# Performance work log

Hardware: AMD Instinct MI355X
Metric: run time of the kernel (lower is better)

## Reference

```python
import jax, jax.numpy as jnp
import numpy as np

N, E, NFEAT, NHID, NCLASS = 50000, 800000, 8, 128, 112
SMOOTH = 0.5          # smoo init arg
NEG_SLOPE_ATT = 0.2   # LeakyReLU slope inside sparse attention (SpGAT convention)
NEG_SLOPE_OUT = 0.01  # F.leaky_relu default in the outer loop
EPS = 1e-16


def setup_inputs() -> dict:
    key = jax.random.key(0)
    ks = jax.random.split(key, 12)
    g = lambda k, shape, s=0.1: jax.random.normal(k, shape, dtype=jnp.float32) * s
    return {
        "x": jax.random.normal(ks[0], (N, NFEAT), dtype=jnp.float32),
        "edge_index": jax.random.randint(ks[1], (2, E), 0, N, dtype=jnp.int64) if jax.config.jax_enable_x64 else jax.random.randint(ks[1], (2, E), 0, N, dtype=jnp.int32),
        "edge_weight": jax.random.uniform(ks[2], (E,), dtype=jnp.float32),
        # ScattterAttentionLayer 1: nfeat -> nhid (weight W, attention vector a split into src/dst halves)
        "W1": g(ks[3], (NFEAT, NHID)),
        "a1_src": g(ks[4], (NHID,)),
        "a1_dst": g(ks[5], (NHID,)),
        # ScattterAttentionLayer 2: nhid -> nhid
        "W2": g(ks[6], (NHID, NHID)),
        "a2_src": g(ks[7], (NHID,)),
        "a2_dst": g(ks[8], (NHID,)),
        # shared BatchNorm1d(nhid)
        "gamma": jnp.ones((NHID,), jnp.float32),
        "beta": jnp.zeros((NHID,), jnp.float32),
        # GC_withres: nhid -> nclass
        "Wg": g(ks[9], (NHID, NCLASS)),
        "bg": jnp.zeros((NCLASS,), jnp.float32),
    }


def scatter_attention(h_in, W, a_src, a_dst, src, dst):
    """Sparse GAT-style scatter attention (SpGraphAttentionLayer math).
    score_ij = exp(-leakyrelu(a_src.h_i + a_dst.h_j)); softmax-normalized per dst node."""
    h = h_in @ W                                   # [N, F]
    f_src = h @ a_src                              # [N]
    f_dst = h @ a_dst                              # [N]
    e = jnp.exp(-jax.nn.leaky_relu(f_src[src] + f_dst[dst], NEG_SLOPE_ATT))  # [E]
    denom = jax.ops.segment_sum(e, dst, num_segments=N) + EPS                # [N]
    num = jax.ops.segment_sum(e[:, None] * h[src], dst, num_segments=N)      # [N, F]
    return num / denom[:, None]


def batchnorm(x, gamma, beta):
    mu = x.mean(axis=0)
    var = x.var(axis=0)
    return (x - mu) * jax.lax.rsqrt(var + 1e-5) * gamma + beta


def reference(x, edge_index, edge_weight, W1, a1_src, a1_dst, W2, a2_src, a2_dst, gamma, beta, Wg, bg):
    src, dst = edge_index[0], edge_index[1]
    # conv loop (nlayers=3 -> two ScattterAttentionLayer convs), shared bn1, leaky_relu; dropout=identity (eval)
    h = scatter_attention(x, W1, a1_src, a1_dst, src, dst)
    h = jax.nn.leaky_relu(batchnorm(h, gamma, beta), NEG_SLOPE_OUT)
    h = scatter_attention(h, W2, a2_src, a2_dst, src, dst)
    h = jax.nn.leaky_relu(batchnorm(h, gamma, beta), NEG_SLOPE_OUT)
    # GC_withres: spmm((smooth*A + I)/(1+smooth), h @ Wg) + bias
    support = h @ Wg                               # [N, nclass]
    w = (SMOOTH / (1.0 + SMOOTH)) * edge_weight    # [E]
    agg = jax.ops.segment_sum(w[:, None] * support[src], dst, num_segments=N)
    return agg + support / (1.0 + SMOOTH) + bg
```

## Files before the change

### kernel.cpp

```cpp
#include <hip/hip_runtime.h>
#include <hip/hip_bf16.h>

#define N_NODES 50000
#define N_EDGES 800000
#define NFEAT   8
#define NHID    128
#define NCLASS  112
#define SEG_EPS 1e-16f
#define BN_EPS  1e-5f
#define CAP     64
#define MACRO_TILES 782
#define NODE_RANGE 6250
#define FILL_CHUNK 2048
#define FILL_CHUNKS 391
#define ATTN_BLOCKS 3125
#define ATTN_ITERS 4
#define Y1_BLOCKS 256

typedef __hip_bfloat16 bf16;
typedef __attribute__((ext_vector_type(8))) short short8;
typedef __attribute__((ext_vector_type(4))) float f32x4;

__device__ __forceinline__ float bfbits2f(unsigned int lo16) {
    union { unsigned int u; float f; } c; c.u = lo16 << 16; return c.f;
}

__device__ __forceinline__ unsigned int pack_bf2(float a, float b) {
    union { unsigned int u; bf16 h[2]; } t;
    t.h[0] = __float2bfloat16(a);
    t.h[1] = __float2bfloat16(b);
    return t.u;
}

__global__ __launch_bounds__(256)
void k_fill_bucket(const int* __restrict__ src, const int* __restrict__ dst,
                   const float* __restrict__ ewt,
                   int* __restrict__ cnt, unsigned int* __restrict__ bucket) {
    const int range = blockIdx.x & 7;
    const int chunk = blockIdx.x >> 3;
    const int lo = range * NODE_RANGE, hi = lo + NODE_RANGE;
    const int e0 = chunk * FILL_CHUNK + threadIdx.x * 8;
    if (e0 >= N_EDGES) return;
    const int4 d0 = *(const int4*)&dst[e0];
    const int4 d1 = *(const int4*)&dst[e0 + 4];
    const int dd[8] = {d0.x, d0.y, d0.z, d0.w, d1.x, d1.y, d1.z, d1.w};
#pragma unroll
    for (int i = 0; i < 8; i++) {
        int d = dd[i];
        if (d < lo || d >= hi) continue;
        int e = e0 + i;
        int slot = atomicAdd(&cnt[d], 1);
        if (slot < CAP) {
            unsigned int iw = (unsigned int)(ewt[e] * 32767.f + 0.5f);
            bucket[d * CAP + slot] = ((unsigned int)src[e] << 15) | iw;
        }
    }
}

__global__ __launch_bounds__(256)
void k_fsfd(const float* __restrict__ x, const float* __restrict__ W1,
            const float* __restrict__ a1s, const float* __restrict__ a1d,
            float* __restrict__ fs, float* __restrict__ fd) {
    __shared__ float sw[16];
    const int t = threadIdx.x, w = t >> 6, lane = t & 63;
#pragma unroll
    for (int dd = 0; dd < 4; dd++) {
        int dot = w + dd * 4;
        int k = dot & 7;
        const float* a = (dot < 8) ? a1s : a1d;
        float v = W1[k * NHID + lane] * a[lane] + W1[k * NHID + 64 + lane] * a[64 + lane];
#pragma unroll
        for (int off = 32; off > 0; off >>= 1) v += __shfl_down(v, off);
        if (lane == 0) sw[dot] = v;
    }
    __syncthreads();
    const int i = blockIdx.x * 256 + t;
    if (i < N_NODES) {
        const float4 x0 = ((const float4*)x)[i * 2];
        const float4 x1 = ((const float4*)x)[i * 2 + 1];
        fs[i] = x0.x*sw[0] + x0.y*sw[1] + x0.z*sw[2] + x0.w*sw[3]
              + x1.x*sw[4] + x1.y*sw[5] + x1.z*sw[6] + x1.w*sw[7];
        fd[i] = x0.x*sw[8] + x0.y*sw[9] + x0.z*sw[10] + x0.w*sw[11]
              + x1.x*sw[12] + x1.y*sw[13] + x1.z*sw[14] + x1.w*sw[15];
    }
}

__global__ __launch_bounds__(256)
void k_sort_gather_x(const int* __restrict__ cnt, unsigned int* __restrict__ bucket,
                     const float* __restrict__ fs, const float* __restrict__ fd,
                     const float* __restrict__ x, float* __restrict__ xaggn) {
    const int d = blockIdx.x * 4 + (threadIdx.x >> 6);
    const int lane = threadIdx.x & 63;
    const int deg = min(cnt[d], CAP);
    unsigned int v = (lane < deg) ? bucket[d * CAP + lane] : 0xFFFFFFFFu;
#pragma unroll
    for (int k = 2; k <= 64; k <<= 1) {
#pragma unroll
        for (int s = k >> 1; s > 0; s >>= 1) {
            unsigned int o = (unsigned int)__shfl_xor((int)v, s);
            bool keepmin = ((lane & s) == 0) == ((lane & k) == 0);
            v = keepmin ? min(v, o) : max(v, o);
        }
    }
    if (lane < deg) bucket[d * CAP + lane] = v;
    const int col = lane & 7, eslot = lane >> 3;
    const float fdd = fd[d];
    float acc = 0.f, den = 0.f;
    for (int base = 0; base < deg; base += 8) {
        int e = base + eslot;
        unsigned int u = (unsigned int)__shfl((int)v, e);
        if (e < deg) {
            int s = u >> 15;
            float f = fs[s] + fdd;
            float lr = f > 0.f ? f : 0.2f * f;
            float c = __expf(-lr);
            den += c;
            acc += c * x[s * NFEAT + col];
        }
    }
#pragma unroll
    for (int off = 8; off < 64; off <<= 1) {
        acc += __shfl_xor(acc, off);
        den += __shfl_xor(den, off);
    }
    if (eslot == 0) xaggn[d * NFEAT + col] = acc / (den + SEG_EPS);
}

__global__ __launch_bounds__(256)
void k_y1_gemm(const float* __restrict__ xaggn, const float* __restrict__ W1,
               bf16* __restrict__ y1, float* __restrict__ Psum, float* __restrict__ Psq) {
    int t = threadIdx.x;
    int r = t >> 7, j = t & 127;
    float w[NFEAT];
#pragma unroll
    for (int k = 0; k < NFEAT; k++) w[k] = W1[k * NHID + j];
    float ls = 0.f, lq = 0.f;
    for (int row = blockIdx.x * 2 + r; row < N_NODES; row += gridDim.x * 2) {
        const float4 x0 = ((const float4*)xaggn)[row * 2];
        const float4 x1 = ((const float4*)xaggn)[row * 2 + 1];
        float v = x0.x*w[0] + x0.y*w[1] + x0.z*w[2] + x0.w*w[3]
                + x1.x*w[4] + x1.y*w[5] + x1.z*w[6] + x1.w*w[7];
        y1[(size_t)row * NHID + j] = __float2bfloat16(v);
        ls += v; lq += v * v;
    }
    __shared__ float sbuf[256];
    sbuf[t] = ls; __syncthreads();
    if (r == 0) Psum[blockIdx.x * 128 + j] = sbuf[j] + sbuf[j + 128];
    __syncthreads();
    sbuf[t] = lq; __syncthreads();
    if (r == 0) Psq[blockIdx.x * 128 + j] = sbuf[j] + sbuf[j + 128];
}

__global__ __launch_bounds__(512)
void k_reduce_full(const float* __restrict__ Psum, const float* __restrict__ Psq,
                   const float* __restrict__ gamma, const float* __restrict__ beta,
                   float* __restrict__ scale, float* __restrict__ shift) {
    int j = threadIdx.x & 127;
    int g = threadIdx.x >> 7;
    float s = 0.f, q = 0.f;
#pragma unroll 8
    for (int b = g * 64; b < g * 64 + 64; b++) {
        s += Psum[b * 128 + j];
        q += Psq[b * 128 + j];
    }
    __shared__ float Ls[4][128], Lq[4][128];
    Ls[g][j] = s; Lq[g][j] = q;
    __syncthreads();
    if (g == 0) {
        float st = ((Ls[0][j] + Ls[1][j]) + Ls[2][j]) + Ls[3][j];
        float qt = ((Lq[0][j] + Lq[1][j]) + Lq[2][j]) + Lq[3][j];
        float mu = st * (1.f / N_NODES);
        float var = qt * (1.f / N_NODES) - mu * mu;
        float rs = rsqrtf(var + BN_EPS);
        float ga = gamma[j];
        scale[j] = rs * ga;
        shift[j] = beta[j] - mu * rs * ga;
    }
}

__global__ __launch_bounds__(256)
void k_reduce_a(const float* __restrict__ Psum, const float* __restrict__ Psq,
                int nIn, int chunk,
                float* __restrict__ Qsum, float* __restrict__ Qsq) {
    int j = threadIdx.x & 127;
    int h = threadIdx.x >> 7;
    int u = blockIdx.x * 2 + h;
    int b0 = u * chunk, b1 = min(b0 + chunk, nIn);
    float s = 0.f, q = 0.f;
#pragma unroll 8
    for (int b = b0; b < b1; b++) {
        s += Psum[b * 128 + j];
        q += Psq[b * 128 + j];
    }
    Qsum[u * 128 + j] = s;
    Qsq[u * 128 + j] = q;
}

__global__ __launch_bounds__(512)
void k_reduce_b(const float* __restrict__ Qsum, const float* __restrict__ Qsq,
                const float* __restrict__ gamma, const float* __restrict__ beta,
                float* __restrict__ scale, float* __restrict__ shift) {
    int j = threadIdx.x & 127;
    int g = threadIdx.x >> 7;
    float s = 0.f, q = 0.f;
#pragma unroll
    for (int u = g * 8; u < g * 8 + 8; u++) {
        s += Qsum[u * 128 + j];
        q += Qsq[u * 128 + j];
    }
    __shared__ float Ls[4][128], Lq[4][128];
    Ls[g][j] = s; Lq[g][j] = q;
    __syncthreads();
    if (g == 0) {
        float st = ((Ls[0][j] + Ls[1][j]) + Ls[2][j]) + Ls[3][j];
        float qt = ((Lq[0][j] + Lq[1][j]) + Lq[2][j]) + Lq[3][j];
        float mu = st * (1.f / N_NODES);
        float var = qt * (1.f / N_NODES) - mu * mu;
        float rs = rsqrtf(var + BN_EPS);
        float ga = gamma[j];
        scale[j] = rs * ga;
        shift[j] = beta[j] - mu * rs * ga;
    }
}

__global__ void k_w2proj(const float* __restrict__ W2,
                         const float* __restrict__ as_, const float* __restrict__ ad_,
                         float* __restrict__ ws_, float* __restrict__ wd_) {
    int k = blockIdx.x, n = threadIdx.x;
    float w = W2[k * NHID + n];
    float vs = w * as_[n], vd = w * ad_[n];
#pragma unroll
    for (int off = 32; off > 0; off >>= 1) { vs += __shfl_down(vs, off); vd += __shfl_down(vd, off); }
    __shared__ float ps[2], pd[2];
    if ((n & 63) == 0) { ps[n >> 6] = vs; pd[n >> 6] = vd; }
    __syncthreads();
    if (n == 0) { ws_[k] = ps[0] + ps[1]; wd_[k] = pd[0] + pd[1]; }
}

template<int NCV, bool ATT>
__global__ __launch_bounds__(256)
void k_gemm_mfma(const bf16* __restrict__ Yin,
                 const float* __restrict__ scale, const float* __restrict__ shift,
                 const float* __restrict__ W,
                 bf16* __restrict__ hout,
                 const float* __restrict__ w2s, const float* __restrict__ w2d,
                 float* __restrict__ fs, float* __restrict__ fd) {
    constexpr int NT = NCV / 16;
    __shared__ bf16 Wt[NCV * 136];
    __shared__ bf16 At[64 * 136];
    const int t = threadIdx.x;
    for (int idx = t; idx < 128 * NCV; idx += 256) {
        int k = idx / NCV, n = idx - k * NCV;
        Wt[n * 136 + k] = __float2bfloat16(W[idx]);
    }
    const int p  = t & 63;
    const int rg = t >> 6;
    const float sc0 = scale[2*p],   sh0 = shift[2*p];
    const float sc1 = scale[2*p+1], sh1 = shift[2*p+1];
    const int lane = t & 63;
    const int m16 = lane & 15;
    const int g = lane >> 4;
    short8 attb[4];
    if constexpr (ATT) {
#pragma unroll
        for (int kk = 0; kk < 4; kk++) {
            union { short8 s; unsigned int u[4]; } pk;
            if (m16 < 2) {
                const float* wv = (m16 == 0) ? w2s : w2d;
                const float4 f0 = *(const float4*)&wv[kk * 32 + g * 8];
                const float4 f1 = *(const float4*)&wv[kk * 32 + g * 8 + 4];
                pk.u[0] = pack_bf2(f0.x, f0.y);
                pk.u[1] = pack_bf2(f0.z, f0.w);
                pk.u[2] = pack_bf2(f1.x, f1.y);
                pk.u[3] = pack_bf2(f1.z, f1.w);
            } else {
                pk.u[0] = pk.u[1] = pk.u[2] = pk.u[3] = 0u;
            }
            attb[kk] = pk.s;
        }
    }
    __syncthreads();

    for (int mt = blockIdx.x; mt < MACRO_TILES; mt += gridDim.x) {
        const int row0 = mt * 64;
#pragma unroll
        for (int i2 = 0; i2 < 16; i2++) {
            int row = rg + i2 * 4;
            int grow = row0 + row;
            unsigned int u = (grow < N_NODES) ? ((const unsigned int*)Yin)[(size_t)grow * 64 + p] : 0u;
            float v0 = bfbits2f(u & 0xFFFF) * sc0 + sh0; v0 = v0 > 0.f ? v0 : 0.01f * v0;
            float v1 = bfbits2f(u >> 16)    * sc1 + sh1; v1 = v1 > 0.f ? v1 : 0.01f * v1;
            *(unsigned int*)&At[row * 136 + 2 * p] = pack_bf2(v0, v1);
        }
        __syncthreads();
        f32x4 acc[NT];
#pragma unroll
        for (int c = 0; c < NT; c++) acc[c] = (f32x4){0.f, 0.f, 0.f, 0.f};
        f32x4 accA = (f32x4){0.f, 0.f, 0.f, 0.f};
#pragma unroll
        for (int kk = 0; kk < 4; kk++) {
            short8 af = *(const short8*)&At[(rg * 16 + m16) * 136 + kk * 32 + g * 8];
#pragma unroll
            for (int c = 0; c < NT; c++) {
                short8 bfr = *(const short8*)&Wt[(c * 16 + m16) * 136 + kk * 32 + g * 8];
                acc[c] = __builtin_amdgcn_mfma_f32_16x16x32_bf16(af, bfr, acc[c], 0, 0, 0);
            }
            if constexpr (ATT)
                accA = __builtin_amdgcn_mfma_f32_16x16x32_bf16(af, attb[kk], accA, 0, 0, 0);
        }
        const int orow = row0 + rg * 16 + g * 4;
#pragma unroll
        for (int c = 0; c < NT; c++) {
#pragma unroll
            for (int r = 0; r < 4; r++) {
                int grow = orow + r;
                if (grow < N_NODES)
                    hout[(size_t)grow * NCV + c * 16 + m16] = __float2bfloat16(acc[c][r]);
            }
        }
        if constexpr (ATT) {
            if (m16 < 2) {
                float* o = (m16 == 0) ? fs : fd;
#pragma unroll
                for (int r = 0; r < 4; r++) {
                    int grow = orow + r;
                    if (grow < N_NODES) o[grow] = accA[r];
                }
            }
        }
        __syncthreads();
    }
}

__global__ __launch_bounds__(256)
void k_gather_attn_bf(const int* __restrict__ cnt, const unsigned int* __restrict__ bucket,
                      const float* __restrict__ fs, const float* __restrict__ fd,
                      const bf16* __restrict__ h, bf16* __restrict__ y,
                      float* __restrict__ Psum, float* __restrict__ Psq) {
    const int q = threadIdx.x >> 6;
    const int j = threadIdx.x & 63;
    __shared__ int s_idx[4][CAP];
    __shared__ float s_e[4][CAP];
    __shared__ float red[4][64][2];
    float ls0 = 0.f, ls1 = 0.f, lq0 = 0.f, lq1 = 0.f;
    for (int it = 0; it < ATTN_ITERS; it++) {
        const int d = (blockIdx.x + it * ATTN_BLOCKS) * 4 + q;
        const int deg = min(cnt[d], CAP);
        const float fdd = fd[d];
        if (j < deg) {
            int s = bucket[d * CAP + j] >> 15;
            float f = fs[s] + fdd;
            float lr = f > 0.f ? f : 0.2f * f;
            s_idx[q][j] = s;
            s_e[q][j] = __expf(-lr);
        }
        float n0 = 0.f, n1 = 0.f, den = 0.f;
#pragma unroll 4
        for (int k = 0; k < deg; k++) {
            float e = s_e[q][k];
            unsigned int u = *(const unsigned int*)&h[(size_t)s_idx[q][k] * NHID + 2 * j];
            den += e;
            n0 += e * bfbits2f(u & 0xFFFF);
            n1 += e * bfbits2f(u >> 16);
        }
        float rsd = 1.f / (den + SEG_EPS);
        float v0 = n0 * rsd, v1 = n1 * rsd;
        ((unsigned int*)y)[(size_t)d * 64 + j] = pack_bf2(v0, v1);
        ls0 += v0; lq0 += v0 * v0;
        ls1 += v1; lq1 += v1 * v1;
    }
    red[q][j][0] = ls0; red[q][j][1] = ls1;
    __syncthreads();
    if (q == 0) {
        float a0 = ((red[0][j][0] + red[1][j][0]) + red[2][j][0]) + red[3][j][0];
        float a1 = ((red[0][j][1] + red[1][j][1]) + red[2][j][1]) + red[3][j][1];
        Psum[blockIdx.x * 128 + 2 * j]     = a0;
        Psum[blockIdx.x * 128 + 2 * j + 1] = a1;
    }
    __syncthreads();
    red[q][j][0] = lq0; red[q][j][1] = lq1;
    __syncthreads();
    if (q == 0) {
        float a0 = ((red[0][j][0] + red[1][j][0]) + red[2][j][0]) + red[3][j][0];
        float a1 = ((red[0][j][1] + red[1][j][1]) + red[2][j][1]) + red[3][j][1];
        Psq[blockIdx.x * 128 + 2 * j]     = a0;
        Psq[blockIdx.x * 128 + 2 * j + 1] = a1;
    }
}

__global__ __launch_bounds__(256)
void k_gather_out_bf(const int* __restrict__ cnt, const unsigned int* __restrict__ bucket,
                     const bf16* __restrict__ sup, const float* __restrict__ bg,
                     float* __restrict__ out) {
    int q = threadIdx.x >> 6;
    int j = threadIdx.x & 63;
    int d = blockIdx.x * 4 + q;
    __shared__ int s_idx[4][CAP];
    __shared__ float s_w[4][CAP];
    int deg = min(cnt[d], CAP);
    if (j < deg) {
        unsigned int b = bucket[d * CAP + j];
        s_idx[q][j] = b >> 15;
        s_w[q][j] = (float)(b & 0x7FFF) * (1.f / (32767.f * 3.f));
    }
    __syncthreads();
    if (j >= NCLASS / 2) return;
    float a0 = 0.f, a1 = 0.f;
#pragma unroll 4
    for (int k = 0; k < deg; k++) {
        float w = s_w[q][k];
        unsigned int u = *(const unsigned int*)&sup[(size_t)s_idx[q][k] * NCLASS + 2 * j];
        a0 += w * bfbits2f(u & 0xFFFF);
        a1 += w * bfbits2f(u >> 16);
    }
    unsigned int us = *(const unsigned int*)&sup[(size_t)d * NCLASS + 2 * j];
    float2 o;
    o.x = a0 + bfbits2f(us & 0xFFFF) * (2.f / 3.f) + bg[2 * j];
    o.y = a1 + bfbits2f(us >> 16)    * (2.f / 3.f) + bg[2 * j + 1];
    *(float2*)&out[(size_t)d * NCLASS + 2 * j] = o;
}

extern "C" void kernel_launch(void* const* d_in, const int* in_sizes, int n_in,
                              void* d_out, int out_size, void* d_ws, size_t ws_size,
                              hipStream_t stream) {
    const float* x    = (const float*)d_in[0];
    const int*   ei   = (const int*)d_in[1];
    const float* ewt  = (const float*)d_in[2];
    const float* W1   = (const float*)d_in[3];
    const float* a1s  = (const float*)d_in[4];
    const float* a1d  = (const float*)d_in[5];
    const float* W2   = (const float*)d_in[6];
    const float* a2s  = (const float*)d_in[7];
    const float* a2d  = (const float*)d_in[8];
    const float* gam  = (const float*)d_in[9];
    const float* bet  = (const float*)d_in[10];
    const float* Wg   = (const float*)d_in[11];
    const float* bg   = (const float*)d_in[12];
    float* out = (float*)d_out;

    const int* src = ei;
    const int* dst = ei + N_EDGES;

    float* ws    = (float*)d_ws;
    bf16*  Yb    = (bf16*)ws;
    bf16*  Hb    = (bf16*)(ws + 3203072);
    unsigned int* bucket = (unsigned int*)(ws + 6403072);
    float* xagg  = ws + 9603072;
    float* fs    = ws + 10003072;
    float* fd    = ws + 10053072;
    int*   cnt   = (int*)(ws + 10103072);
    float* scale = ws + 10153072;
    float* shift = scale + 128;
    float* w2s   = shift + 128;
    float* w2d   = w2s + 128;
    float* Psum  = ws + 10153600;
    float* Psq   = Psum + 400000;
    float* Qsum  = Psq + 400000;
    float* Qsq   = Qsum + 4096;

    hipMemsetAsync(cnt, 0, (size_t)N_NODES * 4, stream);
    k_fill_bucket<<<FILL_CHUNKS * 8, 256, 0, stream>>>(src, dst, ewt, cnt, bucket);

    k_fsfd<<<(N_NODES + 255) / 256, 256, 0, stream>>>(x, W1, a1s, a1d, fs, fd);
    k_sort_gather_x<<<N_NODES / 4, 256, 0, stream>>>(cnt, bucket, fs, fd, x, xagg);
    k_y1_gemm<<<Y1_BLOCKS, 256, 0, stream>>>(xagg, W1, Yb, Psum, Psq);
    k_reduce_full<<<1, 512, 0, stream>>>(Psum, Psq, gam, bet, scale, shift);

    k_w2proj<<<128, 128, 0, stream>>>(W2, a2s, a2d, w2s, w2d);
    k_gemm_mfma<128, true><<<MACRO_TILES, 256, 0, stream>>>(Yb, scale, shift, W2, Hb,
                                                            w2s, w2d, fs, fd);
    k_gather_attn_bf<<<ATTN_BLOCKS, 256, 0, stream>>>(cnt, bucket, fs, fd, Hb, Yb,
                                                      Psum, Psq);
    k_reduce_a<<<16, 256, 0, stream>>>(Psum, Psq, ATTN_BLOCKS, 98, Qsum, Qsq);
    k_reduce_b<<<1, 512, 0, stream>>>(Qsum, Qsq, gam, bet, scale, shift);

    k_gemm_mfma<112, false><<<MACRO_TILES, 256, 0, stream>>>(Yb, scale, shift, Wg, Hb,
                                                             nullptr, nullptr, nullptr, nullptr);
    k_gather_out_bf<<<N_NODES / 4, 256, 0, stream>>>(cnt, bucket, Hb, bg, out);
}
```

Before: 323.7 us.

## Vectorize gathers, remap nodes per XCD, and fuse small launch kernels

Several changes land together. The fill and fs/fd kernels are merged, and so are the BN reduction and the W2 projection, which removes two launches. The gather kernels now read 16-byte rows with four edges in flight per wave instead of one 4-byte word per lane. Block-to-node mapping is changed so each XCD handles a contiguous node range matching the bucket fill partition, aiming for better L2 locality. Layer-2 support is stored with a 128-element stride so 16-byte aligned loads work, the GEMM A-tile load is vectorized, and there is more cross-lane shuffle reduction in exchange.

```diff
diff --git a/kernel.cpp b/kernel.cpp
--- a/kernel.cpp
+++ b/kernel.cpp
@@ -13,13 +13,16 @@
 #define NODE_RANGE 6250
 #define FILL_CHUNK 2048
 #define FILL_CHUNKS 391
-#define ATTN_BLOCKS 3125
-#define ATTN_ITERS 4
+#define FSFD_BLOCKS 196
+#define GATH_GRID 12800
+#define ATT_GRID 3200
+#define ATT_IT 4
 #define Y1_BLOCKS 256
 
 typedef __hip_bfloat16 bf16;
 typedef __attribute__((ext_vector_type(8))) short short8;
 typedef __attribute__((ext_vector_type(4))) float f32x4;
+typedef __attribute__((ext_vector_type(4))) unsigned int u32x4;
 
 __device__ __forceinline__ float bfbits2f(unsigned int lo16) {
     union { unsigned int u; float f; } c; c.u = lo16 << 16; return c.f;
@@ -33,34 +36,34 @@
 }
 
 __global__ __launch_bounds__(256)
-void k_fill_bucket(const int* __restrict__ src, const int* __restrict__ dst,
-                   const float* __restrict__ ewt,
-                   int* __restrict__ cnt, unsigned int* __restrict__ bucket) {
-    const int range = blockIdx.x & 7;
-    const int chunk = blockIdx.x >> 3;
-    const int lo = range * NODE_RANGE, hi = lo + NODE_RANGE;
-    const int e0 = chunk * FILL_CHUNK + threadIdx.x * 8;
-    if (e0 >= N_EDGES) return;
-    const int4 d0 = *(const int4*)&dst[e0];
-    const int4 d1 = *(const int4*)&dst[e0 + 4];
-    const int dd[8] = {d0.x, d0.y, d0.z, d0.w, d1.x, d1.y, d1.z, d1.w};
-#pragma unroll
-    for (int i = 0; i < 8; i++) {
-        int d = dd[i];
-        if (d < lo || d >= hi) continue;
-        int e = e0 + i;
-        int slot = atomicAdd(&cnt[d], 1);
-        if (slot < CAP) {
-            unsigned int iw = (unsigned int)(ewt[e] * 32767.f + 0.5f);
-            bucket[d * CAP + slot] = ((unsigned int)src[e] << 15) | iw;
-        }
-    }
-}
-
-__global__ __launch_bounds__(256)
-void k_fsfd(const float* __restrict__ x, const float* __restrict__ W1,
-            const float* __restrict__ a1s, const float* __restrict__ a1d,
-            float* __restrict__ fs, float* __restrict__ fd) {
+void k_fill_fsfd(const int* __restrict__ src, const int* __restrict__ dst,
+                 const float* __restrict__ ewt,
+                 int* __restrict__ cnt, unsigned int* __restrict__ bucket,
+                 const float* __restrict__ x, const float* __restrict__ W1,
+                 const float* __restrict__ a1s, const float* __restrict__ a1d,
+                 float* __restrict__ fs, float* __restrict__ fd) {
+    if (blockIdx.x < FILL_CHUNKS * 8) {
+        const int range = blockIdx.x & 7;
+        const int chunk = blockIdx.x >> 3;
+        const int lo = range * NODE_RANGE, hi = lo + NODE_RANGE;
+        const int e0 = chunk * FILL_CHUNK + threadIdx.x * 8;
+        if (e0 >= N_EDGES) return;
+        const int4 d0 = *(const int4*)&dst[e0];
+        const int4 d1 = *(const int4*)&dst[e0 + 4];
+        const int dd[8] = {d0.x, d0.y, d0.z, d0.w, d1.x, d1.y, d1.z, d1.w};
+#pragma unroll
+        for (int i = 0; i < 8; i++) {
+            int d = dd[i];
+            if (d < lo || d >= hi) continue;
+            int e = e0 + i;
+            int slot = atomicAdd(&cnt[d], 1);
+            if (slot < CAP) {
+                unsigned int iw = (unsigned int)(ewt[e] * 32767.f + 0.5f);
+                bucket[d * CAP + slot] = ((unsigned int)src[e] << 15) | iw;
+            }
+        }
+        return;
+    }
     __shared__ float sw[16];
     const int t = threadIdx.x, w = t >> 6, lane = t & 63;
 #pragma unroll
@@ -74,7 +77,7 @@
         if (lane == 0) sw[dot] = v;
     }
     __syncthreads();
-    const int i = blockIdx.x * 256 + t;
+    const int i = (blockIdx.x - FILL_CHUNKS * 8) * 256 + t;
     if (i < N_NODES) {
         const float4 x0 = ((const float4*)x)[i * 2];
         const float4 x1 = ((const float4*)x)[i * 2 + 1];
@@ -89,7 +92,11 @@
 void k_sort_gather_x(const int* __restrict__ cnt, unsigned int* __restrict__ bucket,
                      const float* __restrict__ fs, const float* __restrict__ fd,
                      const float* __restrict__ x, float* __restrict__ xaggn) {
-    const int d = blockIdx.x * 4 + (threadIdx.x >> 6);
+    const int xcd = blockIdx.x & 7;
+    const int wb  = blockIdx.x >> 3;
+    const int ni  = wb * 4 + (threadIdx.x >> 6);
+    if (ni >= NODE_RANGE) return;
+    const int d = xcd * NODE_RANGE + ni;
     const int lane = threadIdx.x & 63;
     const int deg = min(cnt[d], CAP);
     unsigned int v = (lane < deg) ? bucket[d * CAP + lane] : 0xFFFFFFFFu;
@@ -103,27 +110,39 @@
         }
     }
     if (lane < deg) bucket[d * CAP + lane] = v;
-    const int col = lane & 7, eslot = lane >> 3;
+    const int epair = lane >> 1;
+    const int half  = lane & 1;
     const float fdd = fd[d];
-    float acc = 0.f, den = 0.f;
-    for (int base = 0; base < deg; base += 8) {
-        int e = base + eslot;
+    float4 acc = {0.f, 0.f, 0.f, 0.f};
+    float den = 0.f;
+    for (int base = 0; base < deg; base += 32) {
+        int e = base + epair;
         unsigned int u = (unsigned int)__shfl((int)v, e);
         if (e < deg) {
             int s = u >> 15;
             float f = fs[s] + fdd;
             float lr = f > 0.f ? f : 0.2f * f;
             float c = __expf(-lr);
-            den += c;
-            acc += c * x[s * NFEAT + col];
-        }
-    }
-#pragma unroll
-    for (int off = 8; off < 64; off <<= 1) {
-        acc += __shfl_xor(acc, off);
-        den += __shfl_xor(den, off);
-    }
-    if (eslot == 0) xaggn[d * NFEAT + col] = acc / (den + SEG_EPS);
+            if (half == 0) den += c;
+            const float4 xv = *(const float4*)&x[s * NFEAT + half * 4];
+            acc.x += c * xv.x; acc.y += c * xv.y; acc.z += c * xv.z; acc.w += c * xv.w;
+        }
+    }
+#pragma unroll
+    for (int off = 2; off < 64; off <<= 1) {
+        acc.x += __shfl_xor(acc.x, off);
+        acc.y += __shfl_xor(acc.y, off);
+        acc.z += __shfl_xor(acc.z, off);
+        acc.w += __shfl_xor(acc.w, off);
+        den   += __shfl_xor(den, off);
+    }
+    den += __shfl_xor(den, 1);
+    if (lane < 2) {
+        float r = 1.f / (den + SEG_EPS);
+        float4 o;
+        o.x = acc.x * r; o.y = acc.y * r; o.z = acc.z * r; o.w = acc.w * r;
+        *(float4*)&xaggn[d * NFEAT + half * 4] = o;
+    }
 }
 
 __global__ __launch_bounds__(256)
@@ -152,30 +171,48 @@
 }
 
 __global__ __launch_bounds__(512)
-void k_reduce_full(const float* __restrict__ Psum, const float* __restrict__ Psq,
-                   const float* __restrict__ gamma, const float* __restrict__ beta,
-                   float* __restrict__ scale, float* __restrict__ shift) {
-    int j = threadIdx.x & 127;
-    int g = threadIdx.x >> 7;
-    float s = 0.f, q = 0.f;
+void k_bn_w2(const float* __restrict__ Psum, const float* __restrict__ Psq,
+             const float* __restrict__ gamma, const float* __restrict__ beta,
+             float* __restrict__ scale, float* __restrict__ shift,
+             const float* __restrict__ W2,
+             const float* __restrict__ as_, const float* __restrict__ ad_,
+             float* __restrict__ ws_, float* __restrict__ wd_) {
+    const int t = threadIdx.x;
+    if (blockIdx.x == 0) {
+        int j = t & 127;
+        int g = t >> 7;
+        float s = 0.f, q = 0.f;
 #pragma unroll 8
-    for (int b = g * 64; b < g * 64 + 64; b++) {
-        s += Psum[b * 128 + j];
-        q += Psq[b * 128 + j];
-    }
-    __shared__ float Ls[4][128], Lq[4][128];
-    Ls[g][j] = s; Lq[g][j] = q;
-    __syncthreads();
-    if (g == 0) {
-        float st = ((Ls[0][j] + Ls[1][j]) + Ls[2][j]) + Ls[3][j];
-        float qt = ((Lq[0][j] + Lq[1][j]) + Lq[2][j]) + Lq[3][j];
-        float mu = st * (1.f / N_NODES);
-        float var = qt * (1.f / N_NODES) - mu * mu;
-        float rs = rsqrtf(var + BN_EPS);
-        float ga = gamma[j];
-        scale[j] = rs * ga;
-        shift[j] = beta[j] - mu * rs * ga;
-    }
+        for (int b = g * 64; b < g * 64 + 64; b++) {
+            s += Psum[b * 128 + j];
+            q += Psq[b * 128 + j];
+        }
+        __shared__ float Ls[4][128], Lq[4][128];
+        Ls[g][j] = s; Lq[g][j] = q;
+        __syncthreads();
+        if (g == 0) {
+            float st = ((Ls[0][j] + Ls[1][j]) + Ls[2][j]) + Ls[3][j];
+            float qt = ((Lq[0][j] + Lq[1][j]) + Lq[2][j]) + Lq[3][j];
+            float mu = st * (1.f / N_NODES);
+            float var = qt * (1.f / N_NODES) - mu * mu;
+            float rs = rsqrtf(var + BN_EPS);
+            float ga = gamma[j];
+            scale[j] = rs * ga;
+            shift[j] = beta[j] - mu * rs * ga;
+        }
+        return;
+    }
+    const int k = (blockIdx.x - 1) * 4 + (t >> 7);
+    const int n = t & 127;
+    float wv = W2[k * NHID + n];
+    float vs = wv * as_[n], vd = wv * ad_[n];
+#pragma unroll
+    for (int off = 32; off > 0; off >>= 1) { vs += __shfl_down(vs, off); vd += __shfl_down(vd, off); }
+    __shared__ float ps[8], pd[8];
+    const int wid = t >> 6;
+    if ((t & 63) == 0) { ps[wid] = vs; pd[wid] = vd; }
+    __syncthreads();
+    if ((t & 127) == 0) { ws_[k] = ps[wid] + ps[wid + 1]; wd_[k] = pd[wid] + pd[wid + 1]; }
 }
 
 __global__ __launch_bounds__(256)
@@ -223,21 +260,7 @@
     }
 }
 
-__global__ void k_w2proj(const float* __restrict__ W2,
-                         const float* __restrict__ as_, const float* __restrict__ ad_,
-                         float* __restrict__ ws_, float* __restrict__ wd_) {
-    int k = blockIdx.x, n = threadIdx.x;
-    float w = W2[k * NHID + n];
-    float vs = w * as_[n], vd = w * ad_[n];
-#pragma unroll
-    for (int off = 32; off > 0; off >>= 1) { vs += __shfl_down(vs, off); vd += __shfl_down(vd, off); }
-    __shared__ float ps[2], pd[2];
-    if ((n & 63) == 0) { ps[n >> 6] = vs; pd[n >> 6] = vd; }
-    __syncthreads();
-    if (n == 0) { ws_[k] = ps[0] + ps[1]; wd_[k] = pd[0] + pd[1]; }
-}
-
-template<int NCV, bool ATT>
+template<int NCV, int OSTRIDE, bool ATT>
 __global__ __launch_bounds__(256)
 void k_gemm_mfma(const bf16* __restrict__ Yin,
                  const float* __restrict__ scale, const float* __restrict__ shift,
@@ -246,20 +269,35 @@
                  const float* __restrict__ w2s, const float* __restrict__ w2d,
                  float* __restrict__ fs, float* __restrict__ fd) {
     constexpr int NT = NCV / 16;
+    constexpr int NC4 = NCV / 4;
     __shared__ bf16 Wt[NCV * 136];
     __shared__ bf16 At[64 * 136];
     const int t = threadIdx.x;
-    for (int idx = t; idx < 128 * NCV; idx += 256) {
-        int k = idx / NCV, n = idx - k * NCV;
-        Wt[n * 136 + k] = __float2bfloat16(W[idx]);
-    }
-    const int p  = t & 63;
-    const int rg = t >> 6;
-    const float sc0 = scale[2*p],   sh0 = shift[2*p];
-    const float sc1 = scale[2*p+1], sh1 = shift[2*p+1];
+    for (int idx = t; idx < 128 * NC4; idx += 256) {
+        int k = idx / NC4, n4 = (idx - k * NC4) * 4;
+        const float4 wv = *(const float4*)&W[k * NCV + n4];
+        Wt[(n4 + 0) * 136 + k] = __float2bfloat16(wv.x);
+        Wt[(n4 + 1) * 136 + k] = __float2bfloat16(wv.y);
+        Wt[(n4 + 2) * 136 + k] = __float2bfloat16(wv.z);
+        Wt[(n4 + 3) * 136 + k] = __float2bfloat16(wv.w);
+    }
+    const int chunk = t & 15;
+    const int rgrp  = t >> 4;
+    float sc[8], sh[8];
+    {
+        const float4 s0 = *(const float4*)&scale[chunk * 8];
+        const float4 s1 = *(const float4*)&scale[chunk * 8 + 4];
+        const float4 h0 = *(const float4*)&shift[chunk * 8];
+        const float4 h1 = *(const float4*)&shift[chunk * 8 + 4];
+        sc[0]=s0.x; sc[1]=s0.y; sc[2]=s0.z; sc[3]=s0.w;
+        sc[4]=s1.x; sc[5]=s1.y; sc[6]=s1.z; sc[7]=s1.w;
+        sh[0]=h0.x; sh[1]=h0.y; sh[2]=h0.z; sh[3]=h0.w;
+        sh[4]=h1.x; sh[5]=h1.y; sh[6]=h1.z; sh[7]=h1.w;
+    }
     const int lane = t & 63;
     const int m16 = lane & 15;
     const int g = lane >> 4;
+    const int rg = t >> 6;
     short8 attb[4];
     if constexpr (ATT) {
 #pragma unroll
@@ -284,13 +322,21 @@
     for (int mt = blockIdx.x; mt < MACRO_TILES; mt += gridDim.x) {
         const int row0 = mt * 64;
 #pragma unroll
-        for (int i2 = 0; i2 < 16; i2++) {
-            int row = rg + i2 * 4;
+        for (int i2 = 0; i2 < 4; i2++) {
+            int row = rgrp + i2 * 16;
             int grow = row0 + row;
-            unsigned int u = (grow < N_NODES) ? ((const unsigned int*)Yin)[(size_t)grow * 64 + p] : 0u;
-            float v0 = bfbits2f(u & 0xFFFF) * sc0 + sh0; v0 = v0 > 0.f ? v0 : 0.01f * v0;
-            float v1 = bfbits2f(u >> 16)    * sc1 + sh1; v1 = v1 > 0.f ? v1 : 0.01f * v1;
-            *(unsigned int*)&At[row * 136 + 2 * p] = pack_bf2(v0, v1);
+            u32x4 u4 = (grow < N_NODES)
+                ? *(const u32x4*)&((const unsigned int*)Yin)[(size_t)grow * 64 + chunk * 4]
+                : (u32x4){0u, 0u, 0u, 0u};
+            u32x4 pk;
+#pragma unroll
+            for (int fq = 0; fq < 4; fq++) {
+                unsigned int u = u4[fq];
+                float v0 = bfbits2f(u & 0xFFFF) * sc[2*fq]   + sh[2*fq];   v0 = v0 > 0.f ? v0 : 0.01f * v0;
+                float v1 = bfbits2f(u >> 16)    * sc[2*fq+1] + sh[2*fq+1]; v1 = v1 > 0.f ? v1 : 0.01f * v1;
+                pk[fq] = pack_bf2(v0, v1);
+            }
+            *(u32x4*)&At[row * 136 + chunk * 8] = pk;
         }
         __syncthreads();
         f32x4 acc[NT];
@@ -315,7 +361,7 @@
             for (int r = 0; r < 4; r++) {
                 int grow = orow + r;
                 if (grow < N_NODES)
-                    hout[(size_t)grow * NCV + c * 16 + m16] = __float2bfloat16(acc[c][r]);
+                    hout[(size_t)grow * OSTRIDE + c * 16 + m16] = __float2bfloat16(acc[c][r]);
             }
         }
         if constexpr (ATT) {
@@ -337,54 +383,92 @@
                       const float* __restrict__ fs, const float* __restrict__ fd,
                       const bf16* __restrict__ h, bf16* __restrict__ y,
                       float* __restrict__ Psum, float* __restrict__ Psq) {
-    const int q = threadIdx.x >> 6;
-    const int j = threadIdx.x & 63;
+    const int xcd = blockIdx.x & 7;
+    const int wb  = blockIdx.x >> 3;
+    const int t = threadIdx.x;
+    const int q = t >> 6;
+    const int lane = t & 63;
+    const int grp = lane >> 4;
+    const int l = lane & 15;
     __shared__ int s_idx[4][CAP];
     __shared__ float s_e[4][CAP];
-    __shared__ float red[4][64][2];
-    float ls0 = 0.f, ls1 = 0.f, lq0 = 0.f, lq1 = 0.f;
-    for (int it = 0; it < ATTN_ITERS; it++) {
-        const int d = (blockIdx.x + it * ATTN_BLOCKS) * 4 + q;
+    __shared__ float sred[4][16][8];
+    float ls[8], lq[8];
+#pragma unroll
+    for (int i = 0; i < 8; i++) { ls[i] = 0.f; lq[i] = 0.f; }
+
+    for (int it = 0; it < ATT_IT; it++) {
+        const int ni = (wb + it * 400) * 4 + q;
+        if (ni >= NODE_RANGE) continue;
+        const int d = xcd * NODE_RANGE + ni;
         const int deg = min(cnt[d], CAP);
         const float fdd = fd[d];
-        if (j < deg) {
-            int s = bucket[d * CAP + j] >> 15;
+        if (lane < deg) {
+            int s = bucket[d * CAP + lane] >> 15;
             float f = fs[s] + fdd;
             float lr = f > 0.f ? f : 0.2f * f;
-            s_idx[q][j] = s;
-            s_e[q][j] = __expf(-lr);
-        }
-        float n0 = 0.f, n1 = 0.f, den = 0.f;
-#pragma unroll 4
-        for (int k = 0; k < deg; k++) {
-            float e = s_e[q][k];
-            unsigned int u = *(const unsigned int*)&h[(size_t)s_idx[q][k] * NHID + 2 * j];
+            s_idx[q][lane] = s;
+            s_e[q][lane] = __expf(-lr);
+        }
+        float a[8];
+#pragma unroll
+        for (int i = 0; i < 8; i++) a[i] = 0.f;
+        float den = 0.f;
+#pragma unroll 2
+        for (int base = 0; base < deg; base += 4) {
+            int k = base + grp;
+            bool ev = k < deg;
+            int kk = ev ? k : 0;
+            float e = ev ? s_e[q][kk] : 0.f;
+            int sidx = s_idx[q][kk];
+            u32x4 u4 = *(const u32x4*)&((const unsigned int*)h)[(size_t)sidx * 64 + l * 4];
             den += e;
-            n0 += e * bfbits2f(u & 0xFFFF);
-            n1 += e * bfbits2f(u >> 16);
-        }
-        float rsd = 1.f / (den + SEG_EPS);
-        float v0 = n0 * rsd, v1 = n1 * rsd;
-        ((unsigned int*)y)[(size_t)d * 64 + j] = pack_bf2(v0, v1);
-        ls0 += v0; lq0 += v0 * v0;
-        ls1 += v1; lq1 += v1 * v1;
-    }
-    red[q][j][0] = ls0; red[q][j][1] = ls1;
-    __syncthreads();
-    if (q == 0) {
-        float a0 = ((red[0][j][0] + red[1][j][0]) + red[2][j][0]) + red[3][j][0];
-        float a1 = ((red[0][j][1] + red[1][j][1]) + red[2][j][1]) + red[3][j][1];
-        Psum[blockIdx.x * 128 + 2 * j]     = a0;
-        Psum[blockIdx.x * 128 + 2 * j + 1] = a1;
-    }
-    __syncthreads();
-    red[q][j][0] = lq0; red[q][j][1] = lq1;
-    __syncthreads();
-    if (q == 0) {
-        float a0 = ((red[0][j][0] + red[1][j][0]) + red[2][j][0]) + red[3][j][0];
-        float a1 = ((red[0][j][1] + red[1][j][1]) + red[2][j][1]) + red[3][j][1];
-        Psq[blockIdx.x * 128 + 2 * j]     = a0;
-        Psq[blockIdx.x * 128 + 2 * j + 1] = a1;
+#pragma unroll
+            for (int fq = 0; fq < 4; fq++) {
+                unsigned int u = u4[fq];
+                a[2*fq]   += e * bfbits2f(u & 0xFFFF);
+                a[2*fq+1] += e * bfbits2f(u >> 16);
+            }
+        }
+#pragma unroll
+        for (int off = 16; off < 64; off <<= 1) {
+#pragma unroll
+            for (int i = 0; i < 8; i++) a[i] += __shfl_xor(a[i], off);
+            den += __shfl_xor(den, off);
+        }
+        float r = 1.f / (den + SEG_EPS);
+        if (lane < 16) {
+            u32x4 pk;
+#pragma unroll
+            for (int fq = 0; fq < 4; fq++) {
+                float v0 = a[2*fq] * r, v1 = a[2*fq+1] * r;
+                pk[fq] = pack_bf2(v0, v1);
+                ls[2*fq] += v0;   lq[2*fq] += v0 * v0;
+                ls[2*fq+1] += v1; lq[2*fq+1] += v1 * v1;
+            }
+            *(u32x4*)&((unsigned int*)y)[(size_t)d * 64 + l * 4] = pk;
+        }
+    }
+    if (lane < 16) {
+#pragma unroll
+        for (int i = 0; i < 8; i++) sred[q][l][i] = ls[i];
+    }
+    __syncthreads();
+    if (t < 128) {
+        int l16 = t >> 3, i8 = t & 7;
+        Psum[blockIdx.x * 128 + t] =
+            ((sred[0][l16][i8] + sred[1][l16][i8]) + sred[2][l16][i8]) + sred[3][l16][i8];
+    }
+    __syncthreads();
+    if (lane < 16) {
+#pragma unroll
+        for (int i = 0; i < 8; i++) sred[q][l][i] = lq[i];
+    }
+    __syncthreads();
+    if (t < 128) {
+        int l16 = t >> 3, i8 = t & 7;
+        Psq[blockIdx.x * 128 + t] =
+            ((sred[0][l16][i8] + sred[1][l16][i8]) + sred[2][l16][i8]) + sred[3][l16][i8];
     }
 }
 
@@ -392,32 +476,63 @@
 void k_gather_out_bf(const int* __restrict__ cnt, const unsigned int* __restrict__ bucket,
                      const bf16* __restrict__ sup, const float* __restrict__ bg,
                      float* __restrict__ out) {
-    int q = threadIdx.x >> 6;
-    int j = threadIdx.x & 63;
-    int d = blockIdx.x * 4 + q;
+    const int xcd = blockIdx.x & 7;
+    const int wb  = blockIdx.x >> 3;
+    const int ni  = wb * 4 + (threadIdx.x >> 6);
+    if (ni >= NODE_RANGE) return;
+    const int d = xcd * NODE_RANGE + ni;
+    const int t = threadIdx.x;
+    const int q = t >> 6;
+    const int lane = t & 63;
+    const int grp = lane >> 4;
+    const int l = lane & 15;
     __shared__ int s_idx[4][CAP];
     __shared__ float s_w[4][CAP];
-    int deg = min(cnt[d], CAP);
-    if (j < deg) {
-        unsigned int b = bucket[d * CAP + j];
-        s_idx[q][j] = b >> 15;
-        s_w[q][j] = (float)(b & 0x7FFF) * (1.f / (32767.f * 3.f));
-    }
-    __syncthreads();
-    if (j >= NCLASS / 2) return;
-    float a0 = 0.f, a1 = 0.f;
-#pragma unroll 4
-    for (int k = 0; k < deg; k++) {
-        float w = s_w[q][k];
-        unsigned int u = *(const unsigned int*)&sup[(size_t)s_idx[q][k] * NCLASS + 2 * j];
-        a0 += w * bfbits2f(u & 0xFFFF);
-        a1 += w * bfbits2f(u >> 16);
-    }
-    unsigned int us = *(const unsigned int*)&sup[(size_t)d * NCLASS + 2 * j];
-    float2 o;
-    o.x = a0 + bfbits2f(us & 0xFFFF) * (2.f / 3.f) + bg[2 * j];
-    o.y = a1 + bfbits2f(us >> 16)    * (2.f / 3.f) + bg[2 * j + 1];
-    *(float2*)&out[(size_t)d * NCLASS + 2 * j] = o;
+    const int deg = min(cnt[d], CAP);
+    if (lane < deg) {
+        unsigned int b = bucket[d * CAP + lane];
+        s_idx[q][lane] = b >> 15;
+        s_w[q][lane] = (float)(b & 0x7FFF) * (1.f / (32767.f * 3.f));
+    }
+    float a[8];
+#pragma unroll
+    for (int i = 0; i < 8; i++) a[i] = 0.f;
+#pragma unroll 2
+    for (int base = 0; base < deg; base += 4) {
+        int k = base + grp;
+        bool ev = k < deg;
+        int kk = ev ? k : 0;
+        float w = ev ? s_w[q][kk] : 0.f;
+        int sidx = s_idx[q][kk];
+        u32x4 u4 = *(const u32x4*)&((const unsigned int*)sup)[(size_t)sidx * 64 + l * 4];
+#pragma unroll
+        for (int fq = 0; fq < 4; fq++) {
+            unsigned int u = u4[fq];
+            a[2*fq]   += w * bfbits2f(u & 0xFFFF);
+            a[2*fq+1] += w * bfbits2f(u >> 16);
+        }
+    }
+#pragma unroll
+    for (int off = 16; off < 64; off <<= 1) {
+#pragma unroll
+        for (int i = 0; i < 8; i++) a[i] += __shfl_xor(a[i], off);
+    }
+    if (l < 14) {
+        u32x4 us = *(const u32x4*)&((const unsigned int*)sup)[(size_t)d * 64 + l * 4];
+        const float4 b0 = *(const float4*)&bg[l * 8];
+        const float4 b1 = *(const float4*)&bg[l * 8 + 4];
+        float4 o0, o1;
+        o0.x = a[0] + bfbits2f(us[0] & 0xFFFF) * (2.f/3.f) + b0.x;
+        o0.y = a[1] + bfbits2f(us[0] >> 16)    * (2.f/3.f) + b0.y;
+        o0.z = a[2] + bfbits2f(us[1] & 0xFFFF) * (2.f/3.f) + b0.z;
+        o0.w = a[3] + bfbits2f(us[1] >> 16)    * (2.f/3.f) + b0.w;
+        o1.x = a[4] + bfbits2f(us[2] & 0xFFFF) * (2.f/3.f) + b1.x;
+        o1.y = a[5] + bfbits2f(us[2] >> 16)    * (2.f/3.f) + b1.y;
+        o1.z = a[6] + bfbits2f(us[3] & 0xFFFF) * (2.f/3.f) + b1.z;
+        o1.w = a[7] + bfbits2f(us[3] >> 16)    * (2.f/3.f) + b1.w;
+        *(float4*)&out[(size_t)d * NCLASS + l * 8]     = o0;
+        *(float4*)&out[(size_t)d * NCLASS + l * 8 + 4] = o1;
+    }
 }
 
 extern "C" void kernel_launch(void* const* d_in, const int* in_sizes, int n_in,
@@ -454,27 +569,27 @@
     float* w2s   = shift + 128;
     float* w2d   = w2s + 128;
     float* Psum  = ws + 10153600;
-    float* Psq   = Psum + 400000;
-    float* Qsum  = Psq + 400000;
+    float* Psq   = Psum + 409600;
+    float* Qsum  = Psq + 409600;
     float* Qsq   = Qsum + 4096;
 
     hipMemsetAsync(cnt, 0, (size_t)N_NODES * 4, stream);
-    k_fill_bucket<<<FILL_CHUNKS * 8, 256, 0, stream>>>(src, dst, ewt, cnt, bucket);
-
-    k_fsfd<<<(N_NODES + 255) / 256, 256, 0, stream>>>(x, W1, a1s, a1d, fs, fd);
-    k_sort_gather_x<<<N_NODES / 4, 256, 0, stream>>>(cnt, bucket, fs, fd, x, xagg);
+    k_fill_fsfd<<<FILL_CHUNKS * 8 + FSFD_BLOCKS, 256, 0, stream>>>(
+        src, dst, ewt, cnt, bucket, x, W1, a1s, a1d, fs, fd);
+
+    k_sort_gather_x<<<GATH_GRID, 256, 0, stream>>>(cnt, bucket, fs, fd, x, xagg);
     k_y1_gemm<<<Y1_BLOCKS, 256, 0, stream>>>(xagg, W1, Yb, Psum, Psq);
-    k_reduce_full<<<1, 512, 0, stream>>>(Psum, Psq, gam, bet, scale, shift);
-
-    k_w2proj<<<128, 128, 0, stream>>>(W2, a2s, a2d, w2s, w2d);
-    k_gemm_mfma<128, true><<<MACRO_TILES, 256, 0, stream>>>(Yb, scale, shift, W2, Hb,
-                                                            w2s, w2d, fs, fd);
-    k_gather_attn_bf<<<ATTN_BLOCKS, 256, 0, stream>>>(cnt, bucket, fs, fd, Hb, Yb,
-                                                      Psum, Psq);
-    k_reduce_a<<<16, 256, 0, stream>>>(Psum, Psq, ATTN_BLOCKS, 98, Qsum, Qsq);
+    k_bn_w2<<<33, 512, 0, stream>>>(Psum, Psq, gam, bet, scale, shift,
+                                    W2, a2s, a2d, w2s, w2d);
+
+    k_gemm_mfma<128, 128, true><<<MACRO_TILES, 256, 0, stream>>>(Yb, scale, shift, W2, Hb,
+                                                                 w2s, w2d, fs, fd);
+    k_gather_attn_bf<<<ATT_GRID, 256, 0, stream>>>(cnt, bucket, fs, fd, Hb, Yb,
+                                                   Psum, Psq);
+    k_reduce_a<<<16, 256, 0, stream>>>(Psum, Psq, ATT_GRID, 100, Qsum, Qsq);
     k_reduce_b<<<1, 512, 0, stream>>>(Qsum, Qsq, gam, bet, scale, shift);
 
-    k_gemm_mfma<112, false><<<MACRO_TILES, 256, 0, stream>>>(Yb, scale, shift, Wg, Hb,
-                                                             nullptr, nullptr, nullptr, nullptr);
-    k_gather_out_bf<<<N_NODES / 4, 256, 0, stream>>>(cnt, bucket, Hb, bg, out);
-}
+    k_gemm_mfma<112, 128, false><<<MACRO_TILES, 256, 0, stream>>>(Yb, scale, shift, Wg, Hb,
+                                                                  nullptr, nullptr, nullptr, nullptr);
+    k_gather_out_bf<<<GATH_GRID, 256, 0, stream>>>(cnt, bucket, Hb, bg, out);
+}
```

Result: no change. 319.8 us (-1.2%).
